# Kernel tuning notes

Measured on AMD Instinct MI355X. Metric: run time of the kernel, lower is better.

Reference implementation:

```python
import jax, jax.numpy as jnp
from jax import lax
import numpy as np

B, T, C, N = 64, 1024, 1, 128  # batch, max seq len, num_conjugates, num_tags


def setup_inputs() -> dict:
    key = jax.random.key(0)
    ks = jax.random.split(key, 6)
    emissions = jax.random.normal(ks[0], (B, T, C, N), dtype=jnp.float32)
    token_sizes = jax.random.randint(ks[1], (B,), T // 2, T + 1)  # ragged lengths in [512, 1024]
    targets = jax.random.randint(ks[2], (B, T), 0, N)
    transitions = jax.random.normal(ks[3], (1, C, N, N), dtype=jnp.float32) * 0.1
    head_transitions = jax.random.normal(ks[4], (1, C, N), dtype=jnp.float32) * 0.1
    last_transitions = jax.random.normal(ks[5], (1, C, N), dtype=jnp.float32) * 0.1
    return dict(emissions=emissions, token_sizes=token_sizes, targets=targets,
                transitions=transitions, head_transitions=head_transitions,
                last_transitions=last_transitions)


def _crf(emissions, token_sizes, targets, transitions, head_transitions, last_transitions):
    # emissions: [B, T, C, N] padded; token_sizes: [B]; targets: [B, T]
    Bq, Tq, Cq, Nq = emissions.shape
    trans = transitions[0]          # [C, N, N]
    head = head_transitions[0]      # [C, N]
    last = last_transitions[0]      # [C, N]

    # ---- log partition (Log semiring forward algorithm; same math as the
    # log-depth semiring tree reduction in crf_partition) ----
    alpha0 = head[None, :, :] + emissions[:, 0]            # [B, C, N]
    emits = jnp.moveaxis(emissions[:, 1:], 1, 0)           # [T-1, B, C, N]
    valid = jnp.arange(1, Tq)[:, None] < token_sizes[None, :]  # [T-1, B]

    def step(alpha, inp):
        emit_t, v = inp
        # alpha[b,c,i] + trans[c,i,j] -> logsumexp over i
        new = jax.nn.logsumexp(alpha[:, :, :, None] + trans[None], axis=2) + emit_t
        return jnp.where(v[:, None, None], new, alpha), None

    alphaT, _ = lax.scan(step, alpha0, (emits, valid))
    log_partitions = jax.nn.logsumexp(alphaT + last[None, :, :], axis=-1)  # [B, C]

    # ---- path score (crf_segment_reduce with Log semiring) ----
    emit_sel = jnp.take_along_axis(emissions, targets[:, :, None, None], axis=3)[..., 0]  # [B, T, C]
    mask = (jnp.arange(Tq)[None, :] < token_sizes[:, None]).astype(emissions.dtype)       # [B, T]
    emit_sum = jnp.sum(emit_sel * mask[:, :, None], axis=1)                               # [B, C]

    prev_t, curr_t = targets[:, :-1], targets[:, 1:]
    trans_sel = trans[:, prev_t, curr_t]                                                  # [C, B, T-1]
    mask2 = (jnp.arange(1, Tq)[None, :] < token_sizes[:, None]).astype(emissions.dtype)   # [B, T-1]
    trans_sum = jnp.sum(trans_sel * mask2[None], axis=-1)                                 # [C, B]

    head_sel = head[:, targets[:, 0]]                                                     # [C, B]
    last_tag = jnp.take_along_axis(targets, (token_sizes - 1)[:, None], axis=1)[:, 0]     # [B]
    last_sel = last[:, last_tag]                                                          # [C, B]

    log_scores = emit_sum + trans_sum.T + head_sel.T + last_sel.T                         # [B, C]
    return jnp.stack([log_partitions, log_scores])  # [2, B, C]


def reference(emissions, token_sizes, targets, transitions, head_transitions, last_transitions):
    return _crf(emissions, token_sizes, targets, transitions, head_transitions, last_transitions)
```

## Files before the change

### kernel.cpp

```cpp
#include <hip/hip_runtime.h>
#include <math.h>

#define Bq 64
#define Tq 1024
#define Nq 128
#define SEG 65
#define NFW (SEG - 1)
#define NBW (SEG - 1)
#define WPC 8
#define LN2 0.6931471805599453f

typedef __attribute__((ext_vector_type(8))) _Float16 half8;
typedef __attribute__((ext_vector_type(2))) _Float16 h2;
typedef __attribute__((ext_vector_type(4))) float f32x4;

union BU { int u[4]; int4 v; half8 h; };
union E8 { int2 v; h2 p[2]; };
union E16 { int2 v2[2]; half8 h; };

__device__ __forceinline__ int pk16(float a, float b) {
    auto p = __builtin_amdgcn_cvt_pkrtz(a, b);
    return *(int*)&p;
}

__device__ __forceinline__ int MMAP(int q, int g, int j) {
    return 16 * (2 * q + (j >> 2)) + 4 * g + (j & 3);
}

__global__ __launch_bounds__(256)
void crf_prep_kernel(const float* __restrict__ em,
                     const float* __restrict__ trans,
                     _Float16* __restrict__ eeh,
                     int4* __restrict__ aF, int4* __restrict__ aB) {
    const int bid = blockIdx.x;
    if (bid < 4096) {
        const size_t i = ((size_t)bid * 256 + threadIdx.x) * 8;
        const float4* src = (const float4*)(em + i);
        float4 x0 = src[0], x1 = src[1];
        BU r;
        r.u[0] = pk16(__expf(x0.x), __expf(x0.y));
        r.u[1] = pk16(__expf(x0.z), __expf(x0.w));
        r.u[2] = pk16(__expf(x1.x), __expf(x1.y));
        r.u[3] = pk16(__expf(x1.z), __expf(x1.w));
        *(int4*)(eeh + i) = r.v;
        return;
    }
    const int fb = bid - 4096;
    const bool fwd = (fb < 8);
    const int kf = (fb & 7) * 4 + (threadIdx.x >> 6);
    const int L = threadIdx.x & 63;
    const int c = L & 15, g = L >> 4;
    const int r = kf >> 2, q = kf & 3;
    BU v;
    #pragma unroll
    for (int j = 0; j < 8; ++j) {
        const int m = MMAP(q, g, j);
        const int n = 16 * r + c;
        const float tv = fwd ? trans[m * Nq + n] : trans[n * Nq + m];
        v.h[j] = (_Float16)__expf(tv);
    }
    (fwd ? aF : aB)[kf * 64 + L] = v.v;
}

__device__ __forceinline__ void fwd_step(
    int k, int lenc, int lo, int hi, int g,
    const _Float16* __restrict__ eeh_c,
    const half8 (&afrag)[32], BU (&bf)[4],
    E8 (&eeCur)[8], E8 (&eeNxt)[8], int& Ecum)
{
    f32x4 acc[8];
    #pragma unroll
    for (int r = 0; r < 8; ++r) {
        f32x4 z = {0.f, 0.f, 0.f, 0.f};
        z = __builtin_amdgcn_mfma_f32_16x16x32_f16(afrag[r*4+0], bf[0].h, z, 0, 0, 0);
        z = __builtin_amdgcn_mfma_f32_16x16x32_f16(afrag[r*4+1], bf[1].h, z, 0, 0, 0);
        z = __builtin_amdgcn_mfma_f32_16x16x32_f16(afrag[r*4+2], bf[2].h, z, 0, 0, 0);
        z = __builtin_amdgcn_mfma_f32_16x16x32_f16(afrag[r*4+3], bf[3].h, z, 0, 0, 0);
        acc[r] = z;
    }
    {
        const int tn = min(lo + k, hi);
        const _Float16* bp = eeh_c + (size_t)tn * Nq;
        #pragma unroll
        for (int r = 0; r < 8; ++r)
            eeNxt[r].v = *(const int2*)(bp + 16*r + 4*g);
    }
    float w[32];
    float mx = 0.f;
    #pragma unroll
    for (int r = 0; r < 8; ++r) {
        #pragma unroll
        for (int i = 0; i < 4; ++i) {
            const float ee = (float)eeCur[r].p[i >> 1][i & 1];
            const float wv = acc[r][i] * ee;
            w[r*4+i] = wv;
            mx = fmaxf(mx, wv);
        }
    }
    mx = fmaxf(mx, __shfl_xor(mx, 16, 64));
    mx = fmaxf(mx, __shfl_xor(mx, 32, 64));
    const int eb = (__float_as_int(mx) >> 23) & 255;
    const float sig = __int_as_float((253 - eb) << 23);
    const bool act = (k <= lenc);
    #pragma unroll
    for (int q = 0; q < 4; ++q) {
        const int n0 = pk16(w[8*q+0]*sig, w[8*q+1]*sig);
        const int n1 = pk16(w[8*q+2]*sig, w[8*q+3]*sig);
        const int n2 = pk16(w[8*q+4]*sig, w[8*q+5]*sig);
        const int n3 = pk16(w[8*q+6]*sig, w[8*q+7]*sig);
        bf[q].u[0] = act ? n0 : bf[q].u[0];
        bf[q].u[1] = act ? n1 : bf[q].u[1];
        bf[q].u[2] = act ? n2 : bf[q].u[2];
        bf[q].u[3] = act ? n3 : bf[q].u[3];
    }
    Ecum += act ? (eb - 126) : 0;
}

__device__ __forceinline__ void bwd_step(
    int k, int lenc, int lo, int hi, int g,
    const _Float16* __restrict__ eeh_c,
    const half8 (&afrag)[32], BU (&bf)[4],
    E16 (&eeCur)[4], E16 (&eeNxt)[4], int& Ecum)
{
    BU beff[4];
    #pragma unroll
    for (int q = 0; q < 4; ++q) beff[q].h = bf[q].h * eeCur[q].h;
    f32x4 acc[8];
    #pragma unroll
    for (int r = 0; r < 8; ++r) {
        f32x4 z = {0.f, 0.f, 0.f, 0.f};
        z = __builtin_amdgcn_mfma_f32_16x16x32_f16(afrag[r*4+0], beff[0].h, z, 0, 0, 0);
        z = __builtin_amdgcn_mfma_f32_16x16x32_f16(afrag[r*4+1], beff[1].h, z, 0, 0, 0);
        z = __builtin_amdgcn_mfma_f32_16x16x32_f16(afrag[r*4+2], beff[2].h, z, 0, 0, 0);
        z = __builtin_amdgcn_mfma_f32_16x16x32_f16(afrag[r*4+3], beff[3].h, z, 0, 0, 0);
        acc[r] = z;
    }
    {
        const int tn = max(hi - k, lo);
        const _Float16* bp = eeh_c + (size_t)tn * Nq;
        #pragma unroll
        for (int q = 0; q < 4; ++q) {
            eeNxt[q].v2[0] = *(const int2*)(bp + 32*q + 4*g);
            eeNxt[q].v2[1] = *(const int2*)(bp + 32*q + 16 + 4*g);
        }
    }
    float mx = 0.f;
    #pragma unroll
    for (int r = 0; r < 8; ++r) {
        #pragma unroll
        for (int i = 0; i < 4; ++i) mx = fmaxf(mx, acc[r][i]);
    }
    mx = fmaxf(mx, __shfl_xor(mx, 16, 64));
    mx = fmaxf(mx, __shfl_xor(mx, 32, 64));
    const int eb = (__float_as_int(mx) >> 23) & 255;
    const float sig = __int_as_float((253 - eb) << 23);
    const bool act = (k <= lenc);
    #pragma unroll
    for (int q = 0; q < 4; ++q) {
        const int n0 = pk16(acc[2*q][0]*sig,   acc[2*q][1]*sig);
        const int n1 = pk16(acc[2*q][2]*sig,   acc[2*q][3]*sig);
        const int n2 = pk16(acc[2*q+1][0]*sig, acc[2*q+1][1]*sig);
        const int n3 = pk16(acc[2*q+1][2]*sig, acc[2*q+1][3]*sig);
        bf[q].u[0] = act ? n0 : bf[q].u[0];
        bf[q].u[1] = act ? n1 : bf[q].u[1];
        bf[q].u[2] = act ? n2 : bf[q].u[2];
        bf[q].u[3] = act ? n3 : bf[q].u[3];
    }
    Ecum += act ? (eb - 126) : 0;
}

__global__ __launch_bounds__(64, 1)
void crf_worker_kernel(const float* __restrict__ emissions,
                       const _Float16* __restrict__ eeh,
                       const int4* __restrict__ aF,
                       const int4* __restrict__ aB,
                       const int* __restrict__ token_sizes,
                       const int* __restrict__ targets,
                       const float* __restrict__ transitions,
                       const float* __restrict__ head,
                       const float* __restrict__ last,
                       float* __restrict__ wsA, float* __restrict__ wsB,
                       float* __restrict__ wsLa, float* __restrict__ wsLb,
                       float* __restrict__ wsS) {
    const int L = threadIdx.x;
    const int bid = blockIdx.x;

    if (bid >= Bq * WPC) {
        const int sb = bid - Bq * WPC;
        const int b = sb >> 2;
        const int j = sb & 3;
        const int tsz = token_sizes[b];
        const int* tg = targets + b * Tq;
        const float* em = emissions + (size_t)b * Tq * Nq;
        float sc = 0.f;
        for (int t = 64 * j + L; t < tsz; t += 256) {
            int cur = tg[t];
            sc += em[(size_t)t * Nq + cur];
            if (t >= 1) sc += transitions[tg[t - 1] * Nq + cur];
        }
        #pragma unroll
        for (int off = 32; off >= 1; off >>= 1)
            sc += __shfl_xor(sc, off, 64);
        if (L == 0) {
            const float extra = (j == 0) ? (head[tg[0]] + last[tg[tsz - 1]]) : 0.f;
            wsS[j * Bq + b] = sc + extra;
        }
        return;
    }

    const int b = bid >> 3;
    const int wv = bid & 7;
    const bool isFwd = (wv < 4);
    const int half_ = wv & 3;
    const int c = L & 15;
    const int g = L >> 4;
    const int s = (isFwd ? 1 : 2) + 16 * half_ + c;

    const float* em_c = emissions + (size_t)b * Tq * Nq;
    const _Float16* eeh_c = eeh + (size_t)b * Tq * Nq;
    const int tsz = token_sizes[b];
    const int nst = tsz - 1;
    const int base = nst / SEG;
    const int rem = nst % SEG;
    const int lo = 1 + (s - 1) * base + min(s - 1, rem);
    const int lenc = base + ((s <= rem) ? 1 : 0);
    const int hi = lo + lenc - 1;
    const int kmax = base + 1;

    half8 afrag[32];
    {
        const int4* asrc = isFwd ? aF : aB;
        #pragma unroll
        for (int kf = 0; kf < 32; ++kf) {
            BU t; t.v = asrc[kf * 64 + L];
            afrag[kf] = t.h;
        }
    }

    BU bf[4];
    float M0c;
    {
        float a0[32];
        float mx = -1e30f;
        #pragma unroll
        for (int q = 0; q < 4; ++q) {
            #pragma unroll
            for (int j2 = 0; j2 < 8; ++j2) {
                const int m = MMAP(q, g, j2);
                float v;
                if (isFwd) v = (s == 1)   ? (head[m] + em_c[m]) : 0.f;
                else       v = (s == SEG) ? last[m]             : 0.f;
                a0[q*8+j2] = v;
                mx = fmaxf(mx, v);
            }
        }
        mx = fmaxf(mx, __shfl_xor(mx, 16, 64));
        mx = fmaxf(mx, __shfl_xor(mx, 32, 64));
        M0c = mx;
        #pragma unroll
        for (int q = 0; q < 4; ++q) {
            #pragma unroll
            for (int p = 0; p < 4; ++p)
                bf[q].u[p] = pk16(__expf(a0[q*8+2*p]   - M0c),
                                  __expf(a0[q*8+2*p+1] - M0c));
        }
    }

    int Ecum = 0;
    int k = 1;
    if (isFwd) {
        E8 eeA[8], eeB8[8];
        const _Float16* bp = eeh_c + (size_t)lo * Nq;
        #pragma unroll
        for (int r = 0; r < 8; ++r) eeA[r].v = *(const int2*)(bp + 16*r + 4*g);
        for (; k + 1 <= kmax; k += 2) {
            fwd_step(k,   lenc, lo, hi, g, eeh_c, afrag, bf, eeA, eeB8, Ecum);
            fwd_step(k+1, lenc, lo, hi, g, eeh_c, afrag, bf, eeB8, eeA, Ecum);
        }
        if (k <= kmax)
            fwd_step(k, lenc, lo, hi, g, eeh_c, afrag, bf, eeA, eeB8, Ecum);
    } else {
        E16 eeA[4], eeB8[4];
        const _Float16* bp = eeh_c + (size_t)hi * Nq;
        #pragma unroll
        for (int q = 0; q < 4; ++q) {
            eeA[q].v2[0] = *(const int2*)(bp + 32*q + 4*g);
            eeA[q].v2[1] = *(const int2*)(bp + 32*q + 16 + 4*g);
        }
        for (; k + 1 <= kmax; k += 2) {
            bwd_step(k,   lenc, lo, hi, g, eeh_c, afrag, bf, eeA, eeB8, Ecum);
            bwd_step(k+1, lenc, lo, hi, g, eeh_c, afrag, bf, eeB8, eeA, Ecum);
        }
        if (k <= kmax)
            bwd_step(k, lenc, lo, hi, g, eeh_c, afrag, bf, eeA, eeB8, Ecum);
    }

    {
        float* dst = isFwd ? (wsA + ((size_t)(s - 1) * Bq + b) * Nq)
                           : (wsB + ((size_t)(s - 2) * Bq + b) * Nq);
        #pragma unroll
        for (int q = 0; q < 4; ++q) {
            f32x4 v0, v1;
            #pragma unroll
            for (int t = 0; t < 4; ++t) { v0[t] = (float)bf[q].h[t]; v1[t] = (float)bf[q].h[4+t]; }
            *(f32x4*)(dst + 32*q + 4*g)      = v0;
            *(f32x4*)(dst + 32*q + 16 + 4*g) = v1;
        }
        if (g == 0) {
            const float led = M0c + (float)Ecum * LN2;
            if (isFwd) wsLa[(s - 1) * Bq + b] = led;
            else       wsLb[(s - 2) * Bq + b] = led;
        }
    }
}

__global__ __launch_bounds__(256)
void crf_combine_kernel(const float* __restrict__ wsA,
                        const float* __restrict__ wsB,
                        const float* __restrict__ wsLa,
                        const float* __restrict__ wsLb,
                        const float* __restrict__ wsS,
                        float* __restrict__ out) {
    const int b = blockIdx.x;
    const int tid = threadIdx.x;
    const int wv = tid >> 6;
    const int l = tid & 63;
    __shared__ float part[4];

    float tot = 0.f;
    for (int s = 2 + wv; s <= SEG - 1; s += 4) {
        const float* bb = wsB + ((size_t)(s - 2) * Bq + b) * Nq;
        const float* aa = wsA + ((size_t)(s - 2) * Bq + b) * Nq;
        float z = bb[l] * aa[l] + bb[l + 64] * aa[l + 64];
        float cc = bb[l] + bb[l + 64];
        #pragma unroll
        for (int off = 32; off >= 1; off >>= 1) {
            z += __shfl_xor(z, off, 64);
            cc += __shfl_xor(cc, off, 64);
        }
        tot += __logf(z) + wsLa[(s - 2) * Bq + b] - __logf(cc);
    }
    if (wv == 0) {
        const float* bb = wsB + ((size_t)(SEG - 2) * Bq + b) * Nq;
        const float* aa = wsA + ((size_t)(SEG - 2) * Bq + b) * Nq;
        float z = bb[l] * aa[l] + bb[l + 64] * aa[l + 64];
        #pragma unroll
        for (int off = 32; off >= 1; off >>= 1)
            z += __shfl_xor(z, off, 64);
        tot += __logf(z) + wsLb[(SEG - 2) * Bq + b] + wsLa[(SEG - 2) * Bq + b];
    }
    if (l == 0) part[wv] = tot;
    __syncthreads();
    if (tid == 0) {
        out[b] = (part[0] + part[1]) + (part[2] + part[3]);
        out[Bq + b] = (wsS[0 * Bq + b] + wsS[1 * Bq + b])
                    + (wsS[2 * Bq + b] + wsS[3 * Bq + b]);
    }
}

extern "C" void kernel_launch(void* const* d_in, const int* in_sizes, int n_in,
                              void* d_out, int out_size, void* d_ws, size_t ws_size,
                              hipStream_t stream) {
    const float* emissions   = (const float*)d_in[0];
    const int*   token_sizes = (const int*)d_in[1];
    const int*   targets     = (const int*)d_in[2];
    const float* transitions = (const float*)d_in[3];
    const float* head        = (const float*)d_in[4];
    const float* last        = (const float*)d_in[5];
    float* out = (float*)d_out;

    char* wp = (char*)d_ws;
    _Float16* eeh = (_Float16*)wp;                       wp += (size_t)Bq * Tq * Nq * 2;
    int4* aF = (int4*)wp;                                wp += 32 * 64 * 16;
    int4* aB = (int4*)wp;                                wp += 32 * 64 * 16;
    float* wsA  = (float*)wp;                            wp += (size_t)NFW * Bq * Nq * 4;
    float* wsB  = (float*)wp;                            wp += (size_t)NBW * Bq * Nq * 4;
    float* wsLa = (float*)wp;                            wp += NFW * Bq * 4;
    float* wsLb = (float*)wp;                            wp += NBW * Bq * 4;
    float* wsS  = (float*)wp;

    crf_prep_kernel<<<4096 + 16, 256, 0, stream>>>(emissions, transitions,
                                                   eeh, aF, aB);
    crf_worker_kernel<<<Bq * WPC + 4 * Bq, 64, 0, stream>>>(
        emissions, eeh, aF, aB, token_sizes, targets, transitions, head, last,
        wsA, wsB, wsLa, wsLb, wsS);
    crf_combine_kernel<<<Bq, 256, 0, stream>>>(wsA, wsB, wsLa, wsLb, wsS, out);
}
```

Baseline: 43.88 us.

## Fuse emission exp/fp16 conversion into recurrence worker and drop prep pass

Removes the separate prep pass that exponentiated all emissions into an fp16 workspace buffer; the worker now loads fp32 emissions directly and computes exp plus fp16 packing inline at each step. This removes a full read-write pass over the emissions tensor and its launch cost, at the price of extra global load bytes and exp work inside the latency-bound serial recurrence. The combine kernel is also widened to 8 waves. Leftover unused shared-memory staging code and fwd_step/bwd_step helpers remain as dead code.

Result: slower. 54.84 us (+25.0%).

```diff
diff --git a/kernel.cpp b/kernel.cpp
--- a/kernel.cpp
+++ b/kernel.cpp
@@ -28,24 +28,9 @@
 }
 
 __global__ __launch_bounds__(256)
-void crf_prep_kernel(const float* __restrict__ em,
-                     const float* __restrict__ trans,
-                     _Float16* __restrict__ eeh,
+void crf_prep_kernel(const float* __restrict__ trans,
                      int4* __restrict__ aF, int4* __restrict__ aB) {
-    const int bid = blockIdx.x;
-    if (bid < 4096) {
-        const size_t i = ((size_t)bid * 256 + threadIdx.x) * 8;
-        const float4* src = (const float4*)(em + i);
-        float4 x0 = src[0], x1 = src[1];
-        BU r;
-        r.u[0] = pk16(__expf(x0.x), __expf(x0.y));
-        r.u[1] = pk16(__expf(x0.z), __expf(x0.w));
-        r.u[2] = pk16(__expf(x1.x), __expf(x1.y));
-        r.u[3] = pk16(__expf(x1.z), __expf(x1.w));
-        *(int4*)(eeh + i) = r.v;
-        return;
-    }
-    const int fb = bid - 4096;
+    const int fb = blockIdx.x;
     const bool fwd = (fb < 8);
     const int kf = (fb & 7) * 4 + (threadIdx.x >> 6);
     const int L = threadIdx.x & 63;
@@ -63,8 +48,8 @@
 }
 
 __device__ __forceinline__ void fwd_step(
-    int k, int lenc, int lo, int hi, int g,
-    const _Float16* __restrict__ eeh_c,
+    int k, int lenc, int g,
+    const _Float16 (&eeL)[16][Nq],
     const half8 (&afrag)[32], BU (&bf)[4],
     E8 (&eeCur)[8], E8 (&eeNxt)[8], int& Ecum)
 {
@@ -79,8 +64,8 @@
         acc[r] = z;
     }
     {
-        const int tn = min(lo + k, hi);
-        const _Float16* bp = eeh_c + (size_t)tn * Nq;
+        const int sl = min(k, lenc - 1);
+        const _Float16* bp = &eeL[sl][0];
         #pragma unroll
         for (int r = 0; r < 8; ++r)
             eeNxt[r].v = *(const int2*)(bp + 16*r + 4*g);
@@ -117,8 +102,8 @@
 }
 
 __device__ __forceinline__ void bwd_step(
-    int k, int lenc, int lo, int hi, int g,
-    const _Float16* __restrict__ eeh_c,
+    int k, int lenc, int g,
+    const _Float16 (&eeL)[16][Nq],
     const half8 (&afrag)[32], BU (&bf)[4],
     E16 (&eeCur)[4], E16 (&eeNxt)[4], int& Ecum)
 {
@@ -136,8 +121,8 @@
         acc[r] = z;
     }
     {
-        const int tn = max(hi - k, lo);
-        const _Float16* bp = eeh_c + (size_t)tn * Nq;
+        const int sl = min(k, lenc - 1);
+        const _Float16* bp = &eeL[sl][0];
         #pragma unroll
         for (int q = 0; q < 4; ++q) {
             eeNxt[q].v2[0] = *(const int2*)(bp + 32*q + 4*g);
@@ -171,7 +156,6 @@
 
 __global__ __launch_bounds__(64, 1)
 void crf_worker_kernel(const float* __restrict__ emissions,
-                       const _Float16* __restrict__ eeh,
                        const int4* __restrict__ aF,
                        const int4* __restrict__ aB,
                        const int* __restrict__ token_sizes,
@@ -185,6 +169,8 @@
     const int L = threadIdx.x;
     const int bid = blockIdx.x;
 
+    __shared__ __align__(16) _Float16 eeL[16][Nq];
+
     if (bid >= Bq * WPC) {
         const int sb = bid - Bq * WPC;
         const int b = sb >> 2;
@@ -217,7 +203,6 @@
     const int s = (isFwd ? 1 : 2) + 16 * half_ + c;
 
     const float* em_c = emissions + (size_t)b * Tq * Nq;
-    const _Float16* eeh_c = eeh + (size_t)b * Tq * Nq;
     const int tsz = token_sizes[b];
     const int nst = tsz - 1;
     const int base = nst / SEG;
@@ -227,6 +212,29 @@
     const int hi = lo + lenc - 1;
     const int kmax = base + 1;
 
+
+    const int kmaxS = 16;
+    {
+        float* myrow = nullptr;
+        (void)myrow;
+        #pragma unroll
+        for (int i = 0; i < kmaxS; ++i) {
+            const int row = isFwd ? min(lo + i, hi) : max(hi - i, lo);
+            const float* bp = em_c + (size_t)row * Nq;
+            int* dst = (int*)&eeL[i][0];
+            if (isFwd) {
+                #pragma unroll
+                for (int r = 0; r < 8; ++r) {
+                    const float2 x = *(const float2*)(bp + 16*r + 4*g + ((L & 1) ? 2 : 0));
+                    dst[(L & 31) * 0 + 0] = 0;
+                    (void)x;
+                }
+            }
+            break;
+        }
+    }
+
+
     half8 afrag[32];
     {
         const int4* asrc = isFwd ? aF : aB;
@@ -270,29 +278,220 @@
     int k = 1;
     if (isFwd) {
         E8 eeA[8], eeB8[8];
-        const _Float16* bp = eeh_c + (size_t)lo * Nq;
-        #pragma unroll
-        for (int r = 0; r < 8; ++r) eeA[r].v = *(const int2*)(bp + 16*r + 4*g);
+        {
+            const float* bp = em_c + (size_t)lo * Nq;
+            #pragma unroll
+            for (int r = 0; r < 8; ++r) {
+                const float2 x = *(const float2*)(bp + 16*r + 4*g + 2*(0));
+                const float2 y = *(const float2*)(bp + 16*r + 4*g + 2);
+                eeA[r].v = make_int2(pk16(__expf(x.x), __expf(x.y)),
+                                     pk16(__expf(y.x), __expf(y.y)));
+            }
+        }
         for (; k + 1 <= kmax; k += 2) {
-            fwd_step(k,   lenc, lo, hi, g, eeh_c, afrag, bf, eeA, eeB8, Ecum);
-            fwd_step(k+1, lenc, lo, hi, g, eeh_c, afrag, bf, eeB8, eeA, Ecum);
-        }
-        if (k <= kmax)
-            fwd_step(k, lenc, lo, hi, g, eeh_c, afrag, bf, eeA, eeB8, Ecum);
+            {
+                f32x4 acc[8];
+                #pragma unroll
+                for (int r = 0; r < 8; ++r) {
+                    f32x4 z = {0.f, 0.f, 0.f, 0.f};
+                    z = __builtin_amdgcn_mfma_f32_16x16x32_f16(afrag[r*4+0], bf[0].h, z, 0, 0, 0);
+                    z = __builtin_amdgcn_mfma_f32_16x16x32_f16(afrag[r*4+1], bf[1].h, z, 0, 0, 0);
+                    z = __builtin_amdgcn_mfma_f32_16x16x32_f16(afrag[r*4+2], bf[2].h, z, 0, 0, 0);
+                    z = __builtin_amdgcn_mfma_f32_16x16x32_f16(afrag[r*4+3], bf[3].h, z, 0, 0, 0);
+                    acc[r] = z;
+                }
+                const int tn = min(lo + k, hi);
+                const float* bp = em_c + (size_t)tn * Nq;
+                #pragma unroll
+                for (int r = 0; r < 8; ++r) {
+                    const float2 x = *(const float2*)(bp + 16*r + 4*g);
+                    const float2 y = *(const float2*)(bp + 16*r + 4*g + 2);
+                    eeB8[r].v = make_int2(pk16(__expf(x.x), __expf(x.y)),
+                                          pk16(__expf(y.x), __expf(y.y)));
+                }
+                float w[32]; float mx = 0.f;
+                #pragma unroll
+                for (int r = 0; r < 8; ++r)
+                    #pragma unroll
+                    for (int i = 0; i < 4; ++i) {
+                        const float ee = (float)eeA[r].p[i >> 1][i & 1];
+                        const float wv2 = acc[r][i] * ee;
+                        w[r*4+i] = wv2; mx = fmaxf(mx, wv2);
+                    }
+                mx = fmaxf(mx, __shfl_xor(mx, 16, 64));
+                mx = fmaxf(mx, __shfl_xor(mx, 32, 64));
+                const int eb = (__float_as_int(mx) >> 23) & 255;
+                const float sig = __int_as_float((253 - eb) << 23);
+                const bool act = (k <= lenc);
+                #pragma unroll
+                for (int q = 0; q < 4; ++q) {
+                    const int n0 = pk16(w[8*q+0]*sig, w[8*q+1]*sig);
+                    const int n1 = pk16(w[8*q+2]*sig, w[8*q+3]*sig);
+                    const int n2 = pk16(w[8*q+4]*sig, w[8*q+5]*sig);
+                    const int n3 = pk16(w[8*q+6]*sig, w[8*q+7]*sig);
+                    bf[0+q].u[0] = act ? n0 : bf[q].u[0];
+                    bf[q].u[1] = act ? n1 : bf[q].u[1];
+                    bf[q].u[2] = act ? n2 : bf[q].u[2];
+                    bf[q].u[3] = act ? n3 : bf[q].u[3];
+                }
+                Ecum += act ? (eb - 126) : 0;
+            }
+            {
+                f32x4 acc[8];
+                #pragma unroll
+                for (int r = 0; r < 8; ++r) {
+                    f32x4 z = {0.f, 0.f, 0.f, 0.f};
+                    z = __builtin_amdgcn_mfma_f32_16x16x32_f16(afrag[r*4+0], bf[0].h, z, 0, 0, 0);
+                    z = __builtin_amdgcn_mfma_f32_16x16x32_f16(afrag[r*4+1], bf[1].h, z, 0, 0, 0);
+                    z = __builtin_amdgcn_mfma_f32_16x16x32_f16(afrag[r*4+2], bf[2].h, z, 0, 0, 0);
+                    z = __builtin_amdgcn_mfma_f32_16x16x32_f16(afrag[r*4+3], bf[3].h, z, 0, 0, 0);
+                    acc[r] = z;
+                }
+                const int tn = min(lo + k + 1, hi);
+                const float* bp = em_c + (size_t)tn * Nq;
+                #pragma unroll
+                for (int r = 0; r < 8; ++r) {
+                    const float2 x = *(const float2*)(bp + 16*r + 4*g);
+                    const float2 y = *(const float2*)(bp + 16*r + 4*g + 2);
+                    eeA[r].v = make_int2(pk16(__expf(x.x), __expf(x.y)),
+                                         pk16(__expf(y.x), __expf(y.y)));
+                }
+                float w[32]; float mx = 0.f;
+                #pragma unroll
+                for (int r = 0; r < 8; ++r)
+                    #pragma unroll
+                    for (int i = 0; i < 4; ++i) {
+                        const float ee = (float)eeB8[r].p[i >> 1][i & 1];
+                        const float wv2 = acc[r][i] * ee;
+                        w[r*4+i] = wv2; mx = fmaxf(mx, wv2);
+                    }
+                mx = fmaxf(mx, __shfl_xor(mx, 16, 64));
+                mx = fmaxf(mx, __shfl_xor(mx, 32, 64));
+                const int eb = (__float_as_int(mx) >> 23) & 255;
+                const float sig = __int_as_float((253 - eb) << 23);
+                const bool act = (k + 1 <= lenc);
+                #pragma unroll
+                for (int q = 0; q < 4; ++q) {
+                    const int n0 = pk16(w[8*q+0]*sig, w[8*q+1]*sig);
+                    const int n1 = pk16(w[8*q+2]*sig, w[8*q+3]*sig);
+                    const int n2 = pk16(w[8*q+4]*sig, w[8*q+5]*sig);
+                    const int n3 = pk16(w[8*q+6]*sig, w[8*q+7]*sig);
+                    bf[q].u[0] = act ? n0 : bf[q].u[0];
+                    bf[q].u[1] = act ? n1 : bf[q].u[1];
+                    bf[q].u[2] = act ? n2 : bf[q].u[2];
+                    bf[q].u[3] = act ? n3 : bf[q].u[3];
+                }
+                Ecum += act ? (eb - 126) : 0;
+            }
+        }
+        if (k <= kmax) {
+            f32x4 acc[8];
+            #pragma unroll
+            for (int r = 0; r < 8; ++r) {
+                f32x4 z = {0.f, 0.f, 0.f, 0.f};
+                z = __builtin_amdgcn_mfma_f32_16x16x32_f16(afrag[r*4+0], bf[0].h, z, 0, 0, 0);
+                z = __builtin_amdgcn_mfma_f32_16x16x32_f16(afrag[r*4+1], bf[1].h, z, 0, 0, 0);
+                z = __builtin_amdgcn_mfma_f32_16x16x32_f16(afrag[r*4+2], bf[2].h, z, 0, 0, 0);
+                z = __builtin_amdgcn_mfma_f32_16x16x32_f16(afrag[r*4+3], bf[3].h, z, 0, 0, 0);
+                acc[r] = z;
+            }
+            float w[32]; float mx = 0.f;
+            #pragma unroll
+            for (int r = 0; r < 8; ++r)
+                #pragma unroll
+                for (int i = 0; i < 4; ++i) {
+                    const float ee = (float)eeA[r].p[i >> 1][i & 1];
+                    const float wv2 = acc[r][i] * ee;
+                    w[r*4+i] = wv2; mx = fmaxf(mx, wv2);
+                }
+            mx = fmaxf(mx, __shfl_xor(mx, 16, 64));
+            mx = fmaxf(mx, __shfl_xor(mx, 32, 64));
+            const int eb = (__float_as_int(mx) >> 23) & 255;
+            const float sig = __int_as_float((253 - eb) << 23);
+            const bool act = (k <= lenc);
+            #pragma unroll
+            for (int q = 0; q < 4; ++q) {
+                const int n0 = pk16(w[8*q+0]*sig, w[8*q+1]*sig);
+                const int n1 = pk16(w[8*q+2]*sig, w[8*q+3]*sig);
+                const int n2 = pk16(w[8*q+4]*sig, w[8*q+5]*sig);
+                const int n3 = pk16(w[8*q+6]*sig, w[8*q+7]*sig);
+                bf[q].u[0] = act ? n0 : bf[q].u[0];
+                bf[q].u[1] = act ? n1 : bf[q].u[1];
+                bf[q].u[2] = act ? n2 : bf[q].u[2];
+                bf[q].u[3] = act ? n3 : bf[q].u[3];
+            }
+            Ecum += act ? (eb - 126) : 0;
+        }
     } else {
         E16 eeA[4], eeB8[4];
-        const _Float16* bp = eeh_c + (size_t)hi * Nq;
-        #pragma unroll
-        for (int q = 0; q < 4; ++q) {
-            eeA[q].v2[0] = *(const int2*)(bp + 32*q + 4*g);
-            eeA[q].v2[1] = *(const int2*)(bp + 32*q + 16 + 4*g);
-        }
-        for (; k + 1 <= kmax; k += 2) {
-            bwd_step(k,   lenc, lo, hi, g, eeh_c, afrag, bf, eeA, eeB8, Ecum);
-            bwd_step(k+1, lenc, lo, hi, g, eeh_c, afrag, bf, eeB8, eeA, Ecum);
-        }
-        if (k <= kmax)
-            bwd_step(k, lenc, lo, hi, g, eeh_c, afrag, bf, eeA, eeB8, Ecum);
+        {
+            const float* bp = em_c + (size_t)hi * Nq;
+            #pragma unroll
+            for (int q = 0; q < 4; ++q) {
+                const float2 x0 = *(const float2*)(bp + 32*q + 4*g);
+                const float2 x1 = *(const float2*)(bp + 32*q + 4*g + 2);
+                const float2 y0 = *(const float2*)(bp + 32*q + 16 + 4*g);
+                const float2 y1 = *(const float2*)(bp + 32*q + 16 + 4*g + 2);
+                eeA[q].v2[0] = make_int2(pk16(__expf(x0.x), __expf(x0.y)),
+                                         pk16(__expf(x1.x), __expf(x1.y)));
+                eeA[q].v2[1] = make_int2(pk16(__expf(y0.x), __expf(y0.y)),
+                                         pk16(__expf(y1.x), __expf(y1.y)));
+            }
+        }
+        for (; k <= kmax; ++k) {
+            BU beff[4];
+            #pragma unroll
+            for (int q = 0; q < 4; ++q) beff[q].h = bf[q].h * eeA[q].h;
+            f32x4 acc[8];
+            #pragma unroll
+            for (int r = 0; r < 8; ++r) {
+                f32x4 z = {0.f, 0.f, 0.f, 0.f};
+                z = __builtin_amdgcn_mfma_f32_16x16x32_f16(afrag[r*4+0], beff[0].h, z, 0, 0, 0);
+                z = __builtin_amdgcn_mfma_f32_16x16x32_f16(afrag[r*4+1], beff[1].h, z, 0, 0, 0);
+                z = __builtin_amdgcn_mfma_f32_16x16x32_f16(afrag[r*4+2], beff[2].h, z, 0, 0, 0);
+                z = __builtin_amdgcn_mfma_f32_16x16x32_f16(afrag[r*4+3], beff[3].h, z, 0, 0, 0);
+                acc[r] = z;
+            }
+            {
+                const int tn = max(hi - k, lo);
+                const float* bp = em_c + (size_t)tn * Nq;
+                #pragma unroll
+                for (int q = 0; q < 4; ++q) {
+                    const float2 x0 = *(const float2*)(bp + 32*q + 4*g);
+                    const float2 x1 = *(const float2*)(bp + 32*q + 4*g + 2);
+                    const float2 y0 = *(const float2*)(bp + 32*q + 16 + 4*g);
+                    const float2 y1 = *(const float2*)(bp + 32*q + 16 + 4*g + 2);
+                    eeB8[q].v2[0] = make_int2(pk16(__expf(x0.x), __expf(x0.y)),
+                                              pk16(__expf(x1.x), __expf(x1.y)));
+                    eeB8[q].v2[1] = make_int2(pk16(__expf(y0.x), __expf(y0.y)),
+                                              pk16(__expf(y1.x), __expf(y1.y)));
+                }
+            }
+            float mx = 0.f;
+            #pragma unroll
+            for (int r = 0; r < 8; ++r)
+                #pragma unroll
+                for (int i = 0; i < 4; ++i) mx = fmaxf(mx, acc[r][i]);
+            mx = fmaxf(mx, __shfl_xor(mx, 16, 64));
+            mx = fmaxf(mx, __shfl_xor(mx, 32, 64));
+            const int eb = (__float_as_int(mx) >> 23) & 255;
+            const float sig = __int_as_float((253 - eb) << 23);
+            const bool act = (k <= lenc);
+            #pragma unroll
+            for (int q = 0; q < 4; ++q) {
+                const int n0 = pk16(acc[2*q][0]*sig,   acc[2*q][1]*sig);
+                const int n1 = pk16(acc[2*q][2]*sig,   acc[2*q][3]*sig);
+                const int n2 = pk16(acc[2*q+1][0]*sig, acc[2*q+1][1]*sig);
+                const int n3 = pk16(acc[2*q+1][2]*sig, acc[2*q+1][3]*sig);
+                bf[q].u[0] = act ? n0 : bf[q].u[0];
+                bf[q].u[1] = act ? n1 : bf[q].u[1];
+                bf[q].u[2] = act ? n2 : bf[q].u[2];
+                bf[q].u[3] = act ? n3 : bf[q].u[3];
+            }
+            Ecum += act ? (eb - 126) : 0;
+            #pragma unroll
+            for (int q = 0; q < 4; ++q) { eeA[q].v2[0] = eeB8[q].v2[0]; eeA[q].v2[1] = eeB8[q].v2[1]; }
+        }
     }
 
     {
@@ -314,7 +513,7 @@
     }
 }
 
-__global__ __launch_bounds__(256)
+__global__ __launch_bounds__(512)
 void crf_combine_kernel(const float* __restrict__ wsA,
                         const float* __restrict__ wsB,
                         const float* __restrict__ wsLa,
@@ -325,10 +524,10 @@
     const int tid = threadIdx.x;
     const int wv = tid >> 6;
     const int l = tid & 63;
-    __shared__ float part[4];
+    __shared__ float part[8];
 
     float tot = 0.f;
-    for (int s = 2 + wv; s <= SEG - 1; s += 4) {
+    for (int s = 2 + wv; s <= SEG - 1; s += 8) {
         const float* bb = wsB + ((size_t)(s - 2) * Bq + b) * Nq;
         const float* aa = wsA + ((size_t)(s - 2) * Bq + b) * Nq;
         float z = bb[l] * aa[l] + bb[l + 64] * aa[l + 64];
@@ -352,7 +551,10 @@
     if (l == 0) part[wv] = tot;
     __syncthreads();
     if (tid == 0) {
-        out[b] = (part[0] + part[1]) + (part[2] + part[3]);
+        float tz = 0.f;
+        #pragma unroll
+        for (int i = 0; i < 8; ++i) tz += part[i];
+        out[b] = tz;
         out[Bq + b] = (wsS[0 * Bq + b] + wsS[1 * Bq + b])
                     + (wsS[2 * Bq + b] + wsS[3 * Bq + b]);
     }
@@ -370,7 +572,6 @@
     float* out = (float*)d_out;
 
     char* wp = (char*)d_ws;
-    _Float16* eeh = (_Float16*)wp;                       wp += (size_t)Bq * Tq * Nq * 2;
     int4* aF = (int4*)wp;                                wp += 32 * 64 * 16;
     int4* aB = (int4*)wp;                                wp += 32 * 64 * 16;
     float* wsA  = (float*)wp;                            wp += (size_t)NFW * Bq * Nq * 4;
@@ -379,10 +580,9 @@
     float* wsLb = (float*)wp;                            wp += NBW * Bq * 4;
     float* wsS  = (float*)wp;
 
-    crf_prep_kernel<<<4096 + 16, 256, 0, stream>>>(emissions, transitions,
-                                                   eeh, aF, aB);
+    crf_prep_kernel<<<16, 256, 0, stream>>>(transitions, aF, aB);
     crf_worker_kernel<<<Bq * WPC + 4 * Bq, 64, 0, stream>>>(
-        emissions, eeh, aF, aB, token_sizes, targets, transitions, head, last,
+        emissions, aF, aB, token_sizes, targets, transitions, head, last,
         wsA, wsB, wsLa, wsLb, wsS);
-    crf_combine_kernel<<<Bq, 256, 0, stream>>>(wsA, wsB, wsLa, wsLb, wsS, out);
-}
+    crf_combine_kernel<<<Bq, 512, 0, stream>>>(wsA, wsB, wsLa, wsLb, wsS, out);
+}
```

## Double segment count per sequence and move path score into prep kernel

Applied to the files above, without the earlier changes.

Splits each sequence into 128 chain segments instead of 64, using 16 wavefronts per batch element instead of 8. This shortens each wave's serial MFMA recurrence chain. The path-score computation moves from extra worker blocks into the prep kernel and writes its output directly, which frees worker slots. In exchange the combine kernel has twice as many segment boundaries to reduce, and the workspace traffic grows.

Result: no change. 43.37 us (-1.2%).

```diff
diff --git a/kernel.cpp b/kernel.cpp
--- a/kernel.cpp
+++ b/kernel.cpp
@@ -4,10 +4,10 @@
 #define Bq 64
 #define Tq 1024
 #define Nq 128
-#define SEG 65
+#define SEG 129
 #define NFW (SEG - 1)
 #define NBW (SEG - 1)
-#define WPC 8
+#define WPC 16
 #define LN2 0.6931471805599453f
 
 typedef __attribute__((ext_vector_type(8))) _Float16 half8;
@@ -30,11 +30,17 @@
 __global__ __launch_bounds__(256)
 void crf_prep_kernel(const float* __restrict__ em,
                      const float* __restrict__ trans,
+                     const int* __restrict__ token_sizes,
+                     const int* __restrict__ targets,
+                     const float* __restrict__ head,
+                     const float* __restrict__ last,
                      _Float16* __restrict__ eeh,
-                     int4* __restrict__ aF, int4* __restrict__ aB) {
+                     int4* __restrict__ aF, int4* __restrict__ aB,
+                     float* __restrict__ out) {
     const int bid = blockIdx.x;
+    const int tid = threadIdx.x;
     if (bid < 4096) {
-        const size_t i = ((size_t)bid * 256 + threadIdx.x) * 8;
+        const size_t i = ((size_t)bid * 256 + tid) * 8;
         const float4* src = (const float4*)(em + i);
         float4 x0 = src[0], x1 = src[1];
         BU r;
@@ -45,21 +51,46 @@
         *(int4*)(eeh + i) = r.v;
         return;
     }
-    const int fb = bid - 4096;
-    const bool fwd = (fb < 8);
-    const int kf = (fb & 7) * 4 + (threadIdx.x >> 6);
-    const int L = threadIdx.x & 63;
-    const int c = L & 15, g = L >> 4;
-    const int r = kf >> 2, q = kf & 3;
-    BU v;
-    #pragma unroll
-    for (int j = 0; j < 8; ++j) {
-        const int m = MMAP(q, g, j);
-        const int n = 16 * r + c;
-        const float tv = fwd ? trans[m * Nq + n] : trans[n * Nq + m];
-        v.h[j] = (_Float16)__expf(tv);
-    }
-    (fwd ? aF : aB)[kf * 64 + L] = v.v;
+    if (bid < 4112) {
+        const int fb = bid - 4096;
+        const bool fwd = (fb < 8);
+        const int kf = (fb & 7) * 4 + (tid >> 6);
+        const int L = tid & 63;
+        const int c = L & 15, g = L >> 4;
+        const int r = kf >> 2, q = kf & 3;
+        BU v;
+        #pragma unroll
+        for (int j = 0; j < 8; ++j) {
+            const int m = MMAP(q, g, j);
+            const int n = 16 * r + c;
+            const float tv = fwd ? trans[m * Nq + n] : trans[n * Nq + m];
+            v.h[j] = (_Float16)__expf(tv);
+        }
+        (fwd ? aF : aB)[kf * 64 + L] = v.v;
+        return;
+    }
+    {
+        const int b = bid - 4112;
+        const int tsz = token_sizes[b];
+        const int* tg = targets + b * Tq;
+        const float* emc = em + (size_t)b * Tq * Nq;
+        float sc = 0.f;
+        for (int t = tid; t < tsz; t += 256) {
+            int cur = tg[t];
+            sc += emc[(size_t)t * Nq + cur];
+            if (t >= 1) sc += trans[tg[t - 1] * Nq + cur];
+        }
+        #pragma unroll
+        for (int off = 32; off >= 1; off >>= 1)
+            sc += __shfl_xor(sc, off, 64);
+        __shared__ float wsum[4];
+        if ((tid & 63) == 0) wsum[tid >> 6] = sc;
+        __syncthreads();
+        if (tid == 0) {
+            float tot = (wsum[0] + wsum[1]) + (wsum[2] + wsum[3]);
+            out[Bq + b] = tot + head[tg[0]] + last[tg[tsz - 1]];
+        }
+    }
 }
 
 __device__ __forceinline__ void fwd_step(
@@ -175,43 +206,17 @@
                        const int4* __restrict__ aF,
                        const int4* __restrict__ aB,
                        const int* __restrict__ token_sizes,
-                       const int* __restrict__ targets,
-                       const float* __restrict__ transitions,
                        const float* __restrict__ head,
                        const float* __restrict__ last,
                        float* __restrict__ wsA, float* __restrict__ wsB,
-                       float* __restrict__ wsLa, float* __restrict__ wsLb,
-                       float* __restrict__ wsS) {
+                       float* __restrict__ wsLa, float* __restrict__ wsLb) {
     const int L = threadIdx.x;
     const int bid = blockIdx.x;
 
-    if (bid >= Bq * WPC) {
-        const int sb = bid - Bq * WPC;
-        const int b = sb >> 2;
-        const int j = sb & 3;
-        const int tsz = token_sizes[b];
-        const int* tg = targets + b * Tq;
-        const float* em = emissions + (size_t)b * Tq * Nq;
-        float sc = 0.f;
-        for (int t = 64 * j + L; t < tsz; t += 256) {
-            int cur = tg[t];
-            sc += em[(size_t)t * Nq + cur];
-            if (t >= 1) sc += transitions[tg[t - 1] * Nq + cur];
-        }
-        #pragma unroll
-        for (int off = 32; off >= 1; off >>= 1)
-            sc += __shfl_xor(sc, off, 64);
-        if (L == 0) {
-            const float extra = (j == 0) ? (head[tg[0]] + last[tg[tsz - 1]]) : 0.f;
-            wsS[j * Bq + b] = sc + extra;
-        }
-        return;
-    }
-
-    const int b = bid >> 3;
-    const int wv = bid & 7;
-    const bool isFwd = (wv < 4);
-    const int half_ = wv & 3;
+    const int b = bid >> 4;
+    const int wv = bid & 15;
+    const bool isFwd = (wv < 8);
+    const int half_ = wv & 7;
     const int c = L & 15;
     const int g = L >> 4;
     const int s = (isFwd ? 1 : 2) + 16 * half_ + c;
@@ -314,21 +319,20 @@
     }
 }
 
-__global__ __launch_bounds__(256)
+__global__ __launch_bounds__(512)
 void crf_combine_kernel(const float* __restrict__ wsA,
                         const float* __restrict__ wsB,
                         const float* __restrict__ wsLa,
                         const float* __restrict__ wsLb,
-                        const float* __restrict__ wsS,
                         float* __restrict__ out) {
     const int b = blockIdx.x;
     const int tid = threadIdx.x;
     const int wv = tid >> 6;
     const int l = tid & 63;
-    __shared__ float part[4];
+    __shared__ float part[8];
 
     float tot = 0.f;
-    for (int s = 2 + wv; s <= SEG - 1; s += 4) {
+    for (int s = 2 + wv; s <= SEG - 1; s += 8) {
         const float* bb = wsB + ((size_t)(s - 2) * Bq + b) * Nq;
         const float* aa = wsA + ((size_t)(s - 2) * Bq + b) * Nq;
         float z = bb[l] * aa[l] + bb[l + 64] * aa[l + 64];
@@ -352,9 +356,10 @@
     if (l == 0) part[wv] = tot;
     __syncthreads();
     if (tid == 0) {
-        out[b] = (part[0] + part[1]) + (part[2] + part[3]);
-        out[Bq + b] = (wsS[0 * Bq + b] + wsS[1 * Bq + b])
-                    + (wsS[2 * Bq + b] + wsS[3 * Bq + b]);
+        float tz = 0.f;
+        #pragma unroll
+        for (int i = 0; i < 8; ++i) tz += part[i];
+        out[b] = tz;
     }
 }
 
@@ -377,12 +382,12 @@
     float* wsB  = (float*)wp;                            wp += (size_t)NBW * Bq * Nq * 4;
     float* wsLa = (float*)wp;                            wp += NFW * Bq * 4;
     float* wsLb = (float*)wp;                            wp += NBW * Bq * 4;
-    float* wsS  = (float*)wp;
-
-    crf_prep_kernel<<<4096 + 16, 256, 0, stream>>>(emissions, transitions,
-                                                   eeh, aF, aB);
-    crf_worker_kernel<<<Bq * WPC + 4 * Bq, 64, 0, stream>>>(
-        emissions, eeh, aF, aB, token_sizes, targets, transitions, head, last,
-        wsA, wsB, wsLa, wsLb, wsS);
-    crf_combine_kernel<<<Bq, 256, 0, stream>>>(wsA, wsB, wsLa, wsLb, wsS, out);
-}
+
+    crf_prep_kernel<<<4096 + 16 + Bq, 256, 0, stream>>>(
+        emissions, transitions, token_sizes, targets, head, last,
+        eeh, aF, aB, out);
+    crf_worker_kernel<<<Bq * WPC, 64, 0, stream>>>(
+        emissions, eeh, aF, aB, token_sizes, head, last,
+        wsA, wsB, wsLa, wsLb);
+    crf_combine_kernel<<<Bq, 512, 0, stream>>>(wsA, wsB, wsLa, wsLb, out);
+}
```
